# Kernel optimization log

Measured on AMD Instinct MI355X. Metric: run time of the kernel, lower is better.

Reference implementation:

```python
import jax, jax.numpy as jnp
import numpy as np

HID = 128  # hardcoded in the original module (hyperparameters['hidden_sizes'])
BETA1, BETA2, ADAM_EPS = 0.9, 0.999, 1e-8  # torch.optim.Adam defaults


def _xavier(k, shape):
    lim = np.sqrt(6.0 / (shape[0] + shape[1]))
    return jax.random.uniform(k, shape, jnp.float32, -lim, lim)


def setup_inputs() -> dict:
    key = jax.random.key(0)
    k0, k1, k2 = jax.random.split(key, 3)
    input_size, output_size = 65536, 4096
    return {
        "x": jax.random.uniform(k0, (input_size,), jnp.float32),
        "W1": _xavier(k1, (input_size, HID)),
        "W2": _xavier(k2, (HID, output_size)),
        "b_in": jnp.zeros((input_size,), jnp.float32),
        "b_h": jnp.zeros((HID,), jnp.float32),
        "b_out": jnp.zeros((output_size,), jnp.float32),
        "hidden0": jnp.zeros((HID,), jnp.float32),
        "output0": jnp.zeros((output_size,), jnp.float32),
        "n_iterations": 256,
        "epsilon": 0.01,
    }


def _drho(s):
    # gradient mask of rho = clamp(s, 0, 1), matching torch clamp backward
    return ((s >= 0.0) & (s <= 1.0)).astype(s.dtype)


def reference(x, W1, W2, b_in, b_h, b_out, hidden0, output0, n_iterations, epsilon):
    r_x = jnp.clip(x, 0.0, 1.0)
    xW1 = r_x @ W1  # [HID], constant across iterations (input is clamped/fixed)

    def adam(p, g, m, v, t1):
        m = BETA1 * m + (1.0 - BETA1) * g
        v = BETA2 * v + (1.0 - BETA2) * g * g
        mhat = m / (1.0 - jnp.power(BETA1, t1))
        vhat = v / (1.0 - jnp.power(BETA2, t1))
        return p - epsilon * mhat / (jnp.sqrt(vhat) + ADAM_EPS), m, v

    def step(carry, t):
        h, o, mh, vh, mo, vo = carry
        r_h = jnp.clip(h, 0.0, 1.0)
        r_o = jnp.clip(o, 0.0, 1.0)
        # analytic dE/dh, dE/do of the quadratic Hopfield energy
        g_h = _drho(h) * (r_h - b_h - xW1 - W2 @ r_o)      # [HID]
        g_o = _drho(o) * (r_o - b_out - r_h @ W2)          # [output_size]
        t1 = t + 1.0
        h, mh, vh = adam(h, g_h, mh, vh, t1)
        o, mo, vo = adam(o, g_o, mo, vo, t1)
        return (h, o, mh, vh, mo, vo), None

    init = (hidden0, output0,
            jnp.zeros_like(hidden0), jnp.zeros_like(hidden0),
            jnp.zeros_like(output0), jnp.zeros_like(output0))
    (h, o, *_), _ = jax.lax.scan(step, init, jnp.arange(n_iterations, dtype=jnp.float32))
    return o
```

## Files before the change

kernel.cpp:

```cpp
#include <hip/hip_runtime.h>
#include <stdint.h>

#define HID   128
#define OUT   4096
#define NWG   8
#define SLICE 512
#define NT    512
#define NXB   128
#define RPX   512

typedef unsigned long long u64;

__device__ __forceinline__ u64 pk(uint32_t tag, float v) {
  return ((u64)tag << 32) | (u64)__float_as_uint(v);
}

__global__ __launch_bounds__(NT, 1) void k_all(
    const float* __restrict__ x,
    const float* __restrict__ W1,
    const float* __restrict__ W2,
    const float* __restrict__ b_h,
    const float* __restrict__ b_out,
    const float* __restrict__ h0,
    const float* __restrict__ o0,
    const int* __restrict__ n_iter_p,
    const float* __restrict__ eps_p,
    u64* __restrict__ pbuf,
    u64* __restrict__ xw1p,
    float* __restrict__ out) {

  __shared__ __attribute__((aligned(16))) float red[8 * SLICE];
  __shared__ __attribute__((aligned(16))) float rh_s[HID];
  __shared__ __attribute__((aligned(16))) float ro_s[SLICE];

  const int t = threadIdx.x;

  if (blockIdx.x >= NWG) {
    const int b = blockIdx.x - NWG;
    const int c4 = (t & 31) * 4;
    const int rseg = t >> 5;
    const int r0 = b * RPX + rseg * 32;
    float4 acc = make_float4(0.f, 0.f, 0.f, 0.f);
#pragma unroll 8
    for (int k = 0; k < 32; ++k) {
      const int r = r0 + k;
      const float rx = fminf(fmaxf(x[r], 0.f), 1.f);
      const float4 wv = *(const float4*)&W1[(size_t)r * HID + c4];
      acc.x = fmaf(rx, wv.x, acc.x); acc.y = fmaf(rx, wv.y, acc.y);
      acc.z = fmaf(rx, wv.z, acc.z); acc.w = fmaf(rx, wv.w, acc.w);
    }
    *(float4*)&red[rseg * HID + c4] = acc;
    __syncthreads();
    if (t < HID) {
      float s = 0.f;
#pragma unroll
      for (int k = 0; k < 16; k += 4)
        s += (red[k*HID + t] + red[(k+1)*HID + t]) + (red[(k+2)*HID + t] + red[(k+3)*HID + t]);
      __hip_atomic_store(&xw1p[b * HID + t], pk(1u, s),
                         __ATOMIC_RELAXED, __HIP_MEMORY_SCOPE_AGENT);
    }
    return;
  }

  const int wg = blockIdx.x;
  const int cg = t & 63;
  const int rg = t >> 6;
  const int n_iter = *n_iter_p;
  const float eps  = *eps_p;

  float w2[16][8];
  {
    const float* wp = W2 + (size_t)(rg * 16) * OUT + wg * SLICE + cg;
#pragma unroll
    for (int r = 0; r < 16; ++r)
#pragma unroll
      for (int k = 0; k < 8; ++k)
        w2[r][k] = wp[(size_t)r * OUT + 64 * k];
  }
#pragma unroll
  for (int r = 0; r < 16; ++r)
    asm volatile("" : "+v"(w2[r][0]), "+v"(w2[r][1]), "+v"(w2[r][2]), "+v"(w2[r][3]),
                      "+v"(w2[r][4]), "+v"(w2[r][5]), "+v"(w2[r][6]), "+v"(w2[r][7]));

  float bhx = 0.f, hh = 0.f, mh = 0.f, vh = 0.f;
  if (t < HID) {
    float s = 0.f;
#pragma unroll 1
    for (int ch = 0; ch < 8; ++ch) {
      u64 v[16];
      for (;;) {
#pragma unroll
        for (int k = 0; k < 16; ++k)
          v[k] = __hip_atomic_load(&xw1p[(ch * 16 + k) * HID + t],
                                   __ATOMIC_RELAXED, __HIP_MEMORY_SCOPE_AGENT);
        uint32_t bad = 0u;
#pragma unroll
        for (int k = 0; k < 16; ++k) bad |= ((uint32_t)(v[k] >> 32)) ^ 1u;
        if (bad == 0u) break;
        __builtin_amdgcn_s_sleep(2);
      }
#pragma unroll
      for (int k = 0; k < 16; ++k) s += __uint_as_float((uint32_t)v[k]);
    }
    bhx = b_h[t] + s;
    hh  = h0[t];
    rh_s[t] = fminf(fmaxf(hh, 0.f), 1.f);
  }
  float oo = o0[wg * SLICE + t];
  float mo = 0.f, vo = 0.f;
  const float bo = b_out[wg * SLICE + t];
  ro_s[t] = fminf(fmaxf(oo, 0.f), 1.f);
  __syncthreads();

  float bp1 = 1.f, bp2 = 1.f;

  for (int it = 0; it < n_iter; ++it) {
    bp1 *= 0.9f; bp2 *= 0.999f;
    const float c1 = 1.f / (1.f - bp1);
    const float c2 = 1.f / (1.f - bp2);
    u64* pb = pbuf + (size_t)(it & 1) * (NWG * HID);
    const uint32_t tag = (uint32_t)(it + 1);

    float aB[16];
    {
      float rov[8];
#pragma unroll
      for (int k = 0; k < 8; ++k) rov[k] = ro_s[cg + 64 * k];
#pragma unroll
      for (int r = 0; r < 16; ++r) {
        float a = w2[r][0] * rov[0];
#pragma unroll
        for (int k = 1; k < 8; ++k) a = fmaf(w2[r][k], rov[k], a);
        aB[r] = a;
      }
    }
    {
#pragma unroll
      for (int r = 0; r < 8; ++r) {
        const float keep = (cg & 32) ? aB[r + 8] : aB[r];
        const float send = (cg & 32) ? aB[r]     : aB[r + 8];
        aB[r] = keep + __shfl_xor(send, 32, 64);
      }
#pragma unroll
      for (int r = 0; r < 4; ++r) {
        const float keep = (cg & 16) ? aB[r + 4] : aB[r];
        const float send = (cg & 16) ? aB[r]     : aB[r + 4];
        aB[r] = keep + __shfl_xor(send, 16, 64);
      }
#pragma unroll
      for (int r = 0; r < 2; ++r) {
        const float keep = (cg & 8) ? aB[r + 2] : aB[r];
        const float send = (cg & 8) ? aB[r]     : aB[r + 2];
        aB[r] = keep + __shfl_xor(send, 8, 64);
      }
      {
        const float keep = (cg & 4) ? aB[1] : aB[0];
        const float send = (cg & 4) ? aB[0] : aB[1];
        aB[0] = keep + __shfl_xor(send, 4, 64);
      }
      aB[0] += __shfl_xor(aB[0], 2, 64);
      aB[0] += __shfl_xor(aB[0], 1, 64);
    }
    if ((cg & 3) == 0) {
      __hip_atomic_store(&pb[wg * HID + rg * 16 + (cg >> 2)], pk(tag, aB[0]),
                         __ATOMIC_RELAXED, __HIP_MEMORY_SCOPE_AGENT);
    }

    {
      float aA[8] = {0.f, 0.f, 0.f, 0.f, 0.f, 0.f, 0.f, 0.f};
#pragma unroll
      for (int r = 0; r < 16; ++r) {
        const float rh = rh_s[rg * 16 + r];
#pragma unroll
        for (int k = 0; k < 8; ++k) aA[k] = fmaf(w2[r][k], rh, aA[k]);
      }
#pragma unroll
      for (int k = 0; k < 8; ++k)
        red[rg * SLICE + cg + 64 * k] = aA[k];
    }
    __syncthreads();

    {
      const float s = ((red[t] + red[SLICE + t]) + (red[2*SLICE + t] + red[3*SLICE + t]))
                    + ((red[4*SLICE + t] + red[5*SLICE + t]) + (red[6*SLICE + t] + red[7*SLICE + t]));
      const float ro_old = fminf(fmaxf(oo, 0.f), 1.f);
      const float g = (oo >= 0.f && oo <= 1.f) ? (ro_old - bo - s) : 0.f;
      mo = 0.9f * mo + 0.1f * g;
      vo = 0.999f * vo + 0.001f * g * g;
      oo -= eps * (mo * c1) / (sqrtf(vo * c2) + 1e-8f);
      ro_s[t] = fminf(fmaxf(oo, 0.f), 1.f);
    }

    if (t < HID) {
      float gv[8];
      for (;;) {
        u64 v[8];
#pragma unroll
        for (int wi = 0; wi < 8; ++wi)
          v[wi] = __hip_atomic_load(&pb[wi * HID + t],
                                    __ATOMIC_RELAXED, __HIP_MEMORY_SCOPE_AGENT);
        uint32_t bad = 0u;
#pragma unroll
        for (int wi = 0; wi < 8; ++wi) bad |= ((uint32_t)(v[wi] >> 32)) ^ tag;
        if (bad == 0u) {
#pragma unroll
          for (int wi = 0; wi < 8; ++wi) gv[wi] = __uint_as_float((uint32_t)v[wi]);
          break;
        }
        __builtin_amdgcn_s_sleep(1);
      }
      const float gsum = ((gv[0] + gv[1]) + (gv[2] + gv[3]))
                       + ((gv[4] + gv[5]) + (gv[6] + gv[7]));
      const float rh_old = fminf(fmaxf(hh, 0.f), 1.f);
      const float g = (hh >= 0.f && hh <= 1.f) ? (rh_old - bhx - gsum) : 0.f;
      mh = 0.9f * mh + 0.1f * g;
      vh = 0.999f * vh + 0.001f * g * g;
      hh -= eps * (mh * c1) / (sqrtf(vh * c2) + 1e-8f);
      rh_s[t] = fminf(fmaxf(hh, 0.f), 1.f);
    }
    __syncthreads();
  }

  out[wg * SLICE + t] = oo;
}

extern "C" void kernel_launch(void* const* d_in, const int* in_sizes, int n_in,
                              void* d_out, int out_size, void* d_ws, size_t ws_size,
                              hipStream_t stream) {
  const float* x     = (const float*)d_in[0];
  const float* W1    = (const float*)d_in[1];
  const float* W2    = (const float*)d_in[2];
  const float* b_h   = (const float*)d_in[4];
  const float* b_out = (const float*)d_in[5];
  const float* h0    = (const float*)d_in[6];
  const float* o0    = (const float*)d_in[7];
  const int*   nit   = (const int*)d_in[8];
  const float* eps   = (const float*)d_in[9];

  u64*   pbuf = (u64*)d_ws;
  u64*   xw1p = (u64*)((char*)d_ws + 16384);
  float* out  = (float*)d_out;

  k_all<<<dim3(NWG + NXB), dim3(NT), 0, stream>>>(x, W1, W2, b_h, b_out, h0, o0,
                                                  nit, eps, pbuf, xw1p, out);
}
```

Measured before the change: 603.3 us.

## Spread hidden-state update across all wavefronts with per-lane partial polling

New measurement: 657.0 us. 1.09x slower.

```diff
diff --git a/kernel.cpp b/kernel.cpp
--- a/kernel.cpp
+++ b/kernel.cpp
@@ -30,8 +30,10 @@
     float* __restrict__ out) {
 
   __shared__ __attribute__((aligned(16))) float red[8 * SLICE];
-  __shared__ __attribute__((aligned(16))) float rh_s[HID];
   __shared__ __attribute__((aligned(16))) float ro_s[SLICE];
+  __shared__ __attribute__((aligned(16))) float rh_w[8][16];
+  __shared__ __attribute__((aligned(16))) float bhx_s[HID];
+  __shared__ __attribute__((aligned(16))) float h0_s[HID];
 
   const int t = threadIdx.x;
 
@@ -65,6 +67,9 @@
   const int wg = blockIdx.x;
   const int cg = t & 63;
   const int rg = t >> 6;
+  const int rloc = cg >> 2;
+  const int q    = cg & 3;
+  const int row  = rg * 16 + rloc;
   const int n_iter = *n_iter_p;
   const float eps  = *eps_p;
 
@@ -82,7 +87,6 @@
     asm volatile("" : "+v"(w2[r][0]), "+v"(w2[r][1]), "+v"(w2[r][2]), "+v"(w2[r][3]),
                       "+v"(w2[r][4]), "+v"(w2[r][5]), "+v"(w2[r][6]), "+v"(w2[r][7]));
 
-  float bhx = 0.f, hh = 0.f, mh = 0.f, vh = 0.f;
   if (t < HID) {
     float s = 0.f;
 #pragma unroll 1
@@ -102,15 +106,19 @@
 #pragma unroll
       for (int k = 0; k < 16; ++k) s += __uint_as_float((uint32_t)v[k]);
     }
-    bhx = b_h[t] + s;
-    hh  = h0[t];
-    rh_s[t] = fminf(fmaxf(hh, 0.f), 1.f);
+    bhx_s[t] = b_h[t] + s;
+    h0_s[t]  = h0[t];
   }
   float oo = o0[wg * SLICE + t];
   float mo = 0.f, vo = 0.f;
   const float bo = b_out[wg * SLICE + t];
   ro_s[t] = fminf(fmaxf(oo, 0.f), 1.f);
   __syncthreads();
+
+  float hh  = h0_s[row];
+  float bhx = bhx_s[row];
+  float mh = 0.f, vh = 0.f;
+  if (q == 0) rh_w[rg][rloc] = fminf(fmaxf(hh, 0.f), 1.f);
 
   float bp1 = 1.f, bp2 = 1.f;
 
@@ -161,8 +169,8 @@
       aB[0] += __shfl_xor(aB[0], 2, 64);
       aB[0] += __shfl_xor(aB[0], 1, 64);
     }
-    if ((cg & 3) == 0) {
-      __hip_atomic_store(&pb[wg * HID + rg * 16 + (cg >> 2)], pk(tag, aB[0]),
+    if (q == 0) {
+      __hip_atomic_store(&pb[wg * HID + row], pk(tag, aB[0]),
                          __ATOMIC_RELAXED, __HIP_MEMORY_SCOPE_AGENT);
     }
 
@@ -170,7 +178,7 @@
       float aA[8] = {0.f, 0.f, 0.f, 0.f, 0.f, 0.f, 0.f, 0.f};
 #pragma unroll
       for (int r = 0; r < 16; ++r) {
-        const float rh = rh_s[rg * 16 + r];
+        const float rh = rh_w[rg][r];
 #pragma unroll
         for (int k = 0; k < 8; ++k) aA[k] = fmaf(w2[r][k], rh, aA[k]);
       }
@@ -191,32 +199,25 @@
       ro_s[t] = fminf(fmaxf(oo, 0.f), 1.f);
     }
 
-    if (t < HID) {
-      float gv[8];
+    {
+      u64 v0, v1;
       for (;;) {
-        u64 v[8];
-#pragma unroll
-        for (int wi = 0; wi < 8; ++wi)
-          v[wi] = __hip_atomic_load(&pb[wi * HID + t],
-                                    __ATOMIC_RELAXED, __HIP_MEMORY_SCOPE_AGENT);
-        uint32_t bad = 0u;
-#pragma unroll
-        for (int wi = 0; wi < 8; ++wi) bad |= ((uint32_t)(v[wi] >> 32)) ^ tag;
-        if (bad == 0u) {
-#pragma unroll
-          for (int wi = 0; wi < 8; ++wi) gv[wi] = __uint_as_float((uint32_t)v[wi]);
-          break;
-        }
-        __builtin_amdgcn_s_sleep(1);
-      }
-      const float gsum = ((gv[0] + gv[1]) + (gv[2] + gv[3]))
-                       + ((gv[4] + gv[5]) + (gv[6] + gv[7]));
+        v0 = __hip_atomic_load(&pb[q * HID + row],
+                               __ATOMIC_RELAXED, __HIP_MEMORY_SCOPE_AGENT);
+        v1 = __hip_atomic_load(&pb[(q + 4) * HID + row],
+                               __ATOMIC_RELAXED, __HIP_MEMORY_SCOPE_AGENT);
+        const bool bad = ((uint32_t)(v0 >> 32) != tag) || ((uint32_t)(v1 >> 32) != tag);
+        if (!__any(bad)) break;
+      }
+      float s2 = __uint_as_float((uint32_t)v0) + __uint_as_float((uint32_t)v1);
+      s2 += __shfl_xor(s2, 1, 64);
+      s2 += __shfl_xor(s2, 2, 64);
       const float rh_old = fminf(fmaxf(hh, 0.f), 1.f);
-      const float g = (hh >= 0.f && hh <= 1.f) ? (rh_old - bhx - gsum) : 0.f;
+      const float g = (hh >= 0.f && hh <= 1.f) ? (rh_old - bhx - s2) : 0.f;
       mh = 0.9f * mh + 0.1f * g;
       vh = 0.999f * vh + 0.001f * g * g;
       hh -= eps * (mh * c1) / (sqrtf(vh * c2) + 1e-8f);
-      rh_s[t] = fminf(fmaxf(hh, 0.f), 1.f);
+      if (q == 0) rh_w[rg][rloc] = fminf(fmaxf(hh, 0.f), 1.f);
     }
     __syncthreads();
   }
```
